# Kernel optimization log

Measured on AMD Instinct MI355X. Metric: run time of the kernel, lower is better.

## Reference

```python
import jax, jax.numpy as jnp
import numpy as np

N_TOKENS = 8192
D_MODEL = 1024
N_EXPERTS = 8
TOP_K = 2


def setup_inputs() -> dict:
    key = jax.random.key(0)
    ks = jax.random.split(key, 4)
    scale = 1.0 / np.sqrt(D_MODEL)
    x = jax.random.normal(ks[0], (N_TOKENS, D_MODEL), dtype=jnp.float32)
    gate_w = jax.random.uniform(ks[1], (N_EXPERTS, D_MODEL), jnp.float32, -scale, scale)
    expert_w = jax.random.uniform(ks[2], (N_EXPERTS, D_MODEL, D_MODEL), jnp.float32, -scale, scale)
    expert_b = jax.random.uniform(ks[3], (N_EXPERTS, D_MODEL), jnp.float32, -scale, scale)
    return {"x": x, "gate_w": gate_w, "expert_w": expert_w, "expert_b": expert_b}


def reference(x, gate_w, expert_w, expert_b):
    # Router: logits [N, E], softmax in fp32, top-k, renormalize over selected.
    router_logits = jnp.einsum('nd,ed->ne', x, gate_w)
    probs = jax.nn.softmax(router_logits.astype(jnp.float32), axis=1)
    rw, sel = jax.lax.top_k(probs, TOP_K)            # [N, K]
    rw = rw / jnp.sum(rw, axis=-1, keepdims=True)

    # Dense combine weights [N, E]: routing weight for selected experts, 0 else.
    n_idx = jnp.arange(x.shape[0])[:, None]
    w_dense = jnp.zeros((x.shape[0], N_EXPERTS), jnp.float32).at[n_idx, sel].set(rw)

    # Compute all experts for all tokens (vectorized equivalent of the
    # gather -> Linear -> weighted scatter-add loop; zero weight for
    # unselected experts reproduces the sparse dispatch exactly).
    # expert_w[e] is torch nn.Linear weight [out, in]: y = x @ W^T + b
    h = jnp.einsum('nd,ehd->neh', x, expert_w) + expert_b[None, :, :]  # [N, E, H]
    final = jnp.einsum('neh,ne->nh', h, w_dense.astype(x.dtype))
    return final, router_logits
```

## Files before the change

kernel.cpp:

```cpp
#include <hip/hip_runtime.h>
#include <hip/hip_bf16.h>
#include <stdint.h>

#define NT 8192
#define DM 1024
#define NE 8
#define MAX_TILES 160
#define SLOTS_MAX 17408
#define NKT (DM / 64)

typedef __bf16 bf16x8 __attribute__((ext_vector_type(8)));
typedef float f32x4 __attribute__((ext_vector_type(4)));

typedef const __attribute__((address_space(1))) void* gp_t;
typedef __attribute__((address_space(3))) void* lp_t;
#define GLDS(g, l) __builtin_amdgcn_global_load_lds((gp_t)(g), (lp_t)(l), 16, 0, 0)

__device__ inline unsigned short f2bf(float f) {
  unsigned int u = __float_as_uint(f);
  unsigned int r = (u + 0x7fffu + ((u >> 16) & 1u)) >> 16;
  return (unsigned short)r;
}
__device__ inline float bf2f(unsigned short u) {
  return __uint_as_float((unsigned int)u << 16);
}

__global__ void prep_kernel(const float* __restrict__ ew, unsigned short* __restrict__ wb,
                            const float* __restrict__ x, const float* __restrict__ gw,
                            float* __restrict__ logits, unsigned short* __restrict__ xb,
                            int* __restrict__ top2e, float* __restrict__ top2w,
                            int* __restrict__ pcount) {
  const int b = blockIdx.x;
  const int t = threadIdx.x;
  if (b < 4096) {
    size_t i = ((size_t)b * 256 + t) * 8;
    float4 a = *(const float4*)(ew + i);
    float4 c = *(const float4*)(ew + i + 4);
    union { unsigned short u[8]; uint4 v; } o;
    o.u[0] = f2bf(a.x); o.u[1] = f2bf(a.y); o.u[2] = f2bf(a.z); o.u[3] = f2bf(a.w);
    o.u[4] = f2bf(c.x); o.u[5] = f2bf(c.y); o.u[6] = f2bf(c.z); o.u[7] = f2bf(c.w);
    *(uint4*)(wb + i) = o.v;
    return;
  }
  __shared__ int lcnt[NE];
  if (t < NE) lcnt[t] = 0;
  __syncthreads();
  const int lane = t & 63;
  const int n = (b - 4096) * 4 + (t >> 6);
  const float* xr = x + (size_t)n * DM;
  float s[NE];
#pragma unroll
  for (int e = 0; e < NE; ++e) s[e] = 0.f;
  for (int c = lane; c < DM; c += 64) {
    float xv = xr[c];
    xb[(size_t)n * DM + c] = f2bf(xv);
#pragma unroll
    for (int e = 0; e < NE; ++e) s[e] += xv * gw[e * DM + c];
  }
#pragma unroll
  for (int e = 0; e < NE; ++e) {
#pragma unroll
    for (int off = 32; off > 0; off >>= 1) s[e] += __shfl_xor(s[e], off);
  }
  if (lane == 0) {
    float m = s[0];
#pragma unroll
    for (int e = 1; e < NE; ++e) m = fmaxf(m, s[e]);
    float p[NE];
#pragma unroll
    for (int e = 0; e < NE; ++e) {
      p[e] = __expf(s[e] - m);
      logits[(size_t)n * NE + e] = s[e];
    }
    int e1 = 0; float b1 = p[0];
#pragma unroll
    for (int e = 1; e < NE; ++e) if (p[e] > b1) { b1 = p[e]; e1 = e; }
    int e2 = -1; float b2 = -1.f;
#pragma unroll
    for (int e = 0; e < NE; ++e) if (e != e1 && p[e] > b2) { b2 = p[e]; e2 = e; }
    float inv = 1.f / (b1 + b2);
    top2e[n * 2 + 0] = e1; top2e[n * 2 + 1] = e2;
    top2w[n * 2 + 0] = b1 * inv; top2w[n * 2 + 1] = b2 * inv;
    atomicAdd(&lcnt[e1], 1);
    atomicAdd(&lcnt[e2], 1);
  }
  __syncthreads();
  if (t < NE) pcount[(b - 4096) * NE + t] = lcnt[t];
}

__global__ void plan_kernel(const int* __restrict__ pcount,
                            int* __restrict__ seg_base, int* __restrict__ counts2,
                            int* __restrict__ tile_e, int* __restrict__ tile_row,
                            int* __restrict__ n_tiles, int* __restrict__ slot_token) {
  __shared__ int lcnt[NE];
  __shared__ int sb[NE + 1], tb[NE + 1], cnt[NE];
  const int t = threadIdx.x;
  if (t < NE) lcnt[t] = 0;
  __syncthreads();
  int s[NE];
#pragma unroll
  for (int e = 0; e < NE; ++e) s[e] = 0;
#pragma unroll
  for (int i = 0; i < 8; ++i) {
    const int* p = pcount + (t + 256 * i) * NE;
#pragma unroll
    for (int e = 0; e < NE; ++e) s[e] += p[e];
  }
#pragma unroll
  for (int e = 0; e < NE; ++e) {
#pragma unroll
    for (int off = 32; off > 0; off >>= 1) s[e] += __shfl_xor(s[e], off);
  }
  if ((t & 63) == 0) {
#pragma unroll
    for (int e = 0; e < NE; ++e) atomicAdd(&lcnt[e], s[e]);
  }
  __syncthreads();
  if (t == 0) {
    int base = 0, tt = 0;
    for (int e = 0; e < NE; ++e) {
      sb[e] = base; tb[e] = tt;
      const int c = lcnt[e];
      cnt[e] = c;
      const int nt = (c + 127) >> 7;
      tt += nt;
      base += nt << 7;
    }
    sb[NE] = base; tb[NE] = tt;
    *n_tiles = tt;
  }
  __syncthreads();
  if (t <= NE) seg_base[t] = sb[t];
  if (t < NE) counts2[t] = 0;
  const int total = tb[NE];
  for (int i = t; i < total; i += 256) {
    int e = 0;
#pragma unroll
    for (int q = 0; q < NE; ++q) if (i >= tb[q + 1]) e = q + 1;
    tile_e[i] = e;
    tile_row[i] = sb[e] + (i - tb[e]) * 128;
  }
  for (int i = t; i < NE * 128; i += 256) {
    const int e = i >> 7, off = i & 127;
    const int pos = sb[e] + cnt[e] + off;
    if (pos < sb[e + 1]) slot_token[pos] = 0;
  }
}

__global__ void scatter_kernel(const int* __restrict__ top2e,
                               const int* __restrict__ seg_base, int* __restrict__ counts2,
                               int* __restrict__ slot_token, int* __restrict__ tok2slot) {
  __shared__ int lcnt[NE], lbase[NE];
  const int t = threadIdx.x;
  if (t < NE) lcnt[t] = 0;
  __syncthreads();
  const int n = blockIdx.x * 256 + t;
  const int e0 = top2e[n * 2 + 0], e1 = top2e[n * 2 + 1];
  const int p0 = atomicAdd(&lcnt[e0], 1);
  const int p1 = atomicAdd(&lcnt[e1], 1);
  __syncthreads();
  if (t < NE) lbase[t] = seg_base[t] + atomicAdd(&counts2[t], lcnt[t]);
  __syncthreads();
  const int q0 = lbase[e0] + p0, q1 = lbase[e1] + p1;
  slot_token[q0] = n; slot_token[q1] = n;
  tok2slot[n * 2 + 0] = q0;
  tok2slot[n * 2 + 1] = q1;
}

__global__ __launch_bounds__(256, 2) void moe_gemm_kernel(
    const unsigned short* __restrict__ xb,
    const unsigned short* __restrict__ wb,
    const float* __restrict__ bias,
    const int* __restrict__ slot_token,
    const int* __restrict__ tile_e, const int* __restrict__ tile_row,
    const int* __restrict__ n_tiles,
    unsigned short* __restrict__ y)
{
  const int bid = blockIdx.x;
  const int swz = (bid & 7) * 160 + (bid >> 3);
  const int bm = swz >> 3;
  const int bn = swz & 7;
  if (bm >= *n_tiles) return;
  const int e = tile_e[bm];
  const int row0 = tile_row[bm];
  const int n0 = bn * 128;

  __shared__ __align__(16) unsigned short lA[2][8192];
  __shared__ __align__(16) unsigned short lB[2][8192];

  const int t = threadIdx.x;
  const int lane = t & 63;
  const int w = t >> 6;
  const int wm = w >> 1, wn = w & 1;

  const int srow = t >> 3;
  const int ss = (t & 7) ^ (srow & 7);
  const unsigned short* asrc[4];
  const unsigned short* bsrc[4];
#pragma unroll
  for (int c = 0; c < 4; ++c) {
    const int lr = c * 32 + srow;
    const int tok = slot_token[row0 + lr];
    asrc[c] = xb + (size_t)tok * DM + ss * 8;
    bsrc[c] = wb + (size_t)e * DM * DM + (size_t)(n0 + lr) * DM + ss * 8;
  }

  f32x4 acc[4][4];
#pragma unroll
  for (int i = 0; i < 4; ++i)
#pragma unroll
    for (int j = 0; j < 4; ++j) acc[i][j] = (f32x4){0.f, 0.f, 0.f, 0.f};

  auto stage = [&](int buf, int kt) {
    const int ko = kt * 64;
#pragma unroll
    for (int c = 0; c < 4; ++c) {
      GLDS(asrc[c] + ko, &lA[buf][c * 2048 + w * 512]);
      GLDS(bsrc[c] + ko, &lB[buf][c * 2048 + w * 512]);
    }
  };

  stage(0, 0);
  stage(1, 1);

  for (int kt = 0; kt < NKT; ++kt) {
    if (kt < NKT - 1) {
      asm volatile("s_waitcnt vmcnt(8)" ::: "memory");
    } else {
      asm volatile("s_waitcnt vmcnt(0)" ::: "memory");
    }
    __builtin_amdgcn_sched_barrier(0);
    __builtin_amdgcn_s_barrier();

    const int cur = kt & 1;
    bf16x8 af[2][4], bf[2][4];
#pragma unroll
    for (int ks = 0; ks < 2; ++ks) {
      const int kb = ks * 64 + (lane >> 4) * 16;
#pragma unroll
      for (int mi = 0; mi < 4; ++mi) {
        const int row = wm * 64 + mi * 16 + (lane & 15);
        af[ks][mi] = *(const bf16x8*)((const char*)lA[cur] + row * 128 + (kb ^ ((row & 7) << 4)));
      }
#pragma unroll
      for (int ni = 0; ni < 4; ++ni) {
        const int row = wn * 64 + ni * 16 + (lane & 15);
        bf[ks][ni] = *(const bf16x8*)((const char*)lB[cur] + row * 128 + (kb ^ ((row & 7) << 4)));
      }
    }
    __builtin_amdgcn_s_setprio(1);
#pragma unroll
    for (int ks = 0; ks < 2; ++ks)
#pragma unroll
      for (int mi = 0; mi < 4; ++mi)
#pragma unroll
        for (int ni = 0; ni < 4; ++ni)
          acc[mi][ni] = __builtin_amdgcn_mfma_f32_16x16x32_bf16(af[ks][mi], bf[ks][ni], acc[mi][ni], 0, 0, 0);
    __builtin_amdgcn_s_setprio(0);

    __builtin_amdgcn_sched_barrier(0);
    __builtin_amdgcn_s_barrier();
    if (kt + 2 < NKT) stage(cur, kt + 2);
  }

  const int cgrp = lane >> 4, ccol = lane & 15;
  float bv[4];
#pragma unroll
  for (int ni = 0; ni < 4; ++ni)
    bv[ni] = bias[e * DM + n0 + wn * 64 + ni * 16 + ccol];
#pragma unroll
  for (int mi = 0; mi < 4; ++mi) {
#pragma unroll
    for (int j = 0; j < 4; ++j) {
      const int r = row0 + wm * 64 + mi * 16 + cgrp * 4 + j;
      unsigned short* yrow = y + (size_t)r * DM + n0 + wn * 64;
#pragma unroll
      for (int ni = 0; ni < 4; ++ni)
        yrow[ni * 16 + ccol] = f2bf(acc[mi][ni][j] + bv[ni]);
    }
  }
}

__global__ void combine_kernel(const unsigned short* __restrict__ y,
                               const int* __restrict__ tok2slot,
                               const float* __restrict__ top2w,
                               float* __restrict__ out) {
  const int n = blockIdx.x;
  const int c = threadIdx.x;
  const int s0 = tok2slot[n * 2 + 0], s1 = tok2slot[n * 2 + 1];
  const float w0 = top2w[n * 2 + 0], w1 = top2w[n * 2 + 1];
  ushort4 a = *(const ushort4*)(y + (size_t)s0 * DM + c * 4);
  ushort4 b = *(const ushort4*)(y + (size_t)s1 * DM + c * 4);
  float4 r;
  r.x = w0 * bf2f(a.x) + w1 * bf2f(b.x);
  r.y = w0 * bf2f(a.y) + w1 * bf2f(b.y);
  r.z = w0 * bf2f(a.z) + w1 * bf2f(b.z);
  r.w = w0 * bf2f(a.w) + w1 * bf2f(b.w);
  *(float4*)(out + (size_t)n * DM + c * 4) = r;
}

extern "C" void kernel_launch(void* const* d_in, const int* in_sizes, int n_in,
                              void* d_out, int out_size, void* d_ws, size_t ws_size,
                              hipStream_t stream) {
  const float* x  = (const float*)d_in[0];
  const float* gw = (const float*)d_in[1];
  const float* ew = (const float*)d_in[2];
  const float* eb = (const float*)d_in[3];
  float* out    = (float*)d_out;
  float* logits = out + (size_t)NT * DM;

  char* ws = (char*)d_ws;
  int*   counts2    = (int*)(ws + 64);
  int*   seg_base   = (int*)(ws + 128);
  int*   n_tiles    = (int*)(ws + 192);
  int*   tile_e     = (int*)(ws + 256);
  int*   tile_row   = (int*)(ws + 1024);
  int*   top2e      = (int*)(ws + 2048);
  float* top2w      = (float*)(ws + 67584);
  int*   slot_token = (int*)(ws + 133120);
  int*   tok2slot   = (int*)(ws + 202752);
  int*   pcount     = (int*)(ws + 268288);
  unsigned short* xb = (unsigned short*)(ws + 335872);
  unsigned short* wb = (unsigned short*)(ws + 335872 + 16777216);
  unsigned short* y  = (unsigned short*)(ws + 335872 + 2 * 16777216);

  prep_kernel<<<4096 + NT / 4, 256, 0, stream>>>(ew, wb, x, gw, logits, xb,
                                                 top2e, top2w, pcount);
  plan_kernel<<<1, 256, 0, stream>>>(pcount, seg_base, counts2, tile_e, tile_row,
                                     n_tiles, slot_token);
  scatter_kernel<<<NT / 256, 256, 0, stream>>>(top2e, seg_base, counts2, slot_token, tok2slot);
  moe_gemm_kernel<<<MAX_TILES * 8, 256, 0, stream>>>(xb, wb, eb, slot_token,
                                                     tile_e, tile_row, n_tiles, y);
  combine_kernel<<<NT, 256, 0, stream>>>(y, tok2slot, top2w, out);
}
```

Baseline: 99.10 us.

## Switch expert GEMM to 128x256 tiles with 32x32x16 MFMA and K=32 stages

```diff
diff --git a/kernel.cpp b/kernel.cpp
--- a/kernel.cpp
+++ b/kernel.cpp
@@ -7,10 +7,11 @@
 #define NE 8
 #define MAX_TILES 160
 #define SLOTS_MAX 17408
-#define NKT (DM / 64)
+#define NKT 32
 
 typedef __bf16 bf16x8 __attribute__((ext_vector_type(8)));
 typedef float f32x4 __attribute__((ext_vector_type(4)));
+typedef float f32x16 __attribute__((ext_vector_type(16)));
 
 typedef const __attribute__((address_space(1))) void* gp_t;
 typedef __attribute__((address_space(3))) void* lp_t;
@@ -177,55 +178,61 @@
     unsigned short* __restrict__ y)
 {
   const int bid = blockIdx.x;
-  const int swz = (bid & 7) * 160 + (bid >> 3);
-  const int bm = swz >> 3;
-  const int bn = swz & 7;
+  const int swz = (bid & 7) * 80 + (bid >> 3);
+  const int bm = swz >> 2;
+  const int bn = swz & 3;
   if (bm >= *n_tiles) return;
   const int e = tile_e[bm];
   const int row0 = tile_row[bm];
-  const int n0 = bn * 128;
-
-  __shared__ __align__(16) unsigned short lA[2][8192];
+  const int n0 = bn * 256;
+
+  __shared__ __align__(16) unsigned short lA[2][4096];
   __shared__ __align__(16) unsigned short lB[2][8192];
 
   const int t = threadIdx.x;
   const int lane = t & 63;
   const int w = t >> 6;
-  const int wm = w >> 1, wn = w & 1;
-
-  const int srow = t >> 3;
-  const int ss = (t & 7) ^ (srow & 7);
-  const unsigned short* asrc[4];
+
+  const int sS = (t & 7) ^ ((t >> 3) & 7);
+  const unsigned short* asrc[2];
   const unsigned short* bsrc[4];
 #pragma unroll
+  for (int c = 0; c < 2; ++c) {
+    const int lr = c * 64 + ((t >> 3) << 1) + (sS >> 2);
+    const int tok = slot_token[row0 + lr];
+    asrc[c] = xb + (size_t)tok * DM + (sS & 3) * 8;
+  }
+#pragma unroll
   for (int c = 0; c < 4; ++c) {
-    const int lr = c * 32 + srow;
-    const int tok = slot_token[row0 + lr];
-    asrc[c] = xb + (size_t)tok * DM + ss * 8;
-    bsrc[c] = wb + (size_t)e * DM * DM + (size_t)(n0 + lr) * DM + ss * 8;
-  }
-
-  f32x4 acc[4][4];
+    const int lr = c * 64 + ((t >> 3) << 1) + (sS >> 2);
+    bsrc[c] = wb + (size_t)e * DM * DM + (size_t)(n0 + lr) * DM + (sS & 3) * 8;
+  }
+
+  f32x16 acc[4][2];
 #pragma unroll
   for (int i = 0; i < 4; ++i)
 #pragma unroll
-    for (int j = 0; j < 4; ++j) acc[i][j] = (f32x4){0.f, 0.f, 0.f, 0.f};
+    for (int j = 0; j < 2; ++j)
+#pragma unroll
+      for (int v = 0; v < 16; ++v) acc[i][j][v] = 0.f;
 
   auto stage = [&](int buf, int kt) {
-    const int ko = kt * 64;
-#pragma unroll
-    for (int c = 0; c < 4; ++c) {
-      GLDS(asrc[c] + ko, &lA[buf][c * 2048 + w * 512]);
-      GLDS(bsrc[c] + ko, &lB[buf][c * 2048 + w * 512]);
-    }
+    const int ko = kt * 32;
+    GLDS(asrc[0] + ko, &lA[buf][t * 8]);
+    GLDS(asrc[1] + ko, &lA[buf][2048 + t * 8]);
+#pragma unroll
+    for (int c = 0; c < 4; ++c)
+      GLDS(bsrc[c] + ko, &lB[buf][c * 2048 + t * 8]);
   };
 
   stage(0, 0);
   stage(1, 1);
 
+  const int l31 = lane & 31;
+  const int khalf = lane >> 5;
   for (int kt = 0; kt < NKT; ++kt) {
     if (kt < NKT - 1) {
-      asm volatile("s_waitcnt vmcnt(8)" ::: "memory");
+      asm volatile("s_waitcnt vmcnt(6)" ::: "memory");
     } else {
       asm volatile("s_waitcnt vmcnt(0)" ::: "memory");
     }
@@ -233,29 +240,31 @@
     __builtin_amdgcn_s_barrier();
 
     const int cur = kt & 1;
-    bf16x8 af[2][4], bf[2][4];
-#pragma unroll
-    for (int ks = 0; ks < 2; ++ks) {
-      const int kb = ks * 64 + (lane >> 4) * 16;
-#pragma unroll
-      for (int mi = 0; mi < 4; ++mi) {
-        const int row = wm * 64 + mi * 16 + (lane & 15);
-        af[ks][mi] = *(const bf16x8*)((const char*)lA[cur] + row * 128 + (kb ^ ((row & 7) << 4)));
+    bf16x8 af[2][4], bf[2][2];
+#pragma unroll
+    for (int kg = 0; kg < 2; ++kg) {
+      const int q = kg * 2 + khalf;
+#pragma unroll
+      for (int mb = 0; mb < 4; ++mb) {
+        const int r = mb * 32 + l31;
+        const int off = (r >> 1) * 128 + (((((r & 1) << 2) | q) ^ ((r >> 1) & 7)) << 4);
+        af[kg][mb] = *(const bf16x8*)((const char*)lA[cur] + off);
       }
 #pragma unroll
-      for (int ni = 0; ni < 4; ++ni) {
-        const int row = wn * 64 + ni * 16 + (lane & 15);
-        bf[ks][ni] = *(const bf16x8*)((const char*)lB[cur] + row * 128 + (kb ^ ((row & 7) << 4)));
+      for (int nb = 0; nb < 2; ++nb) {
+        const int r = w * 64 + nb * 32 + l31;
+        const int off = (r >> 1) * 128 + (((((r & 1) << 2) | q) ^ ((r >> 1) & 7)) << 4);
+        bf[kg][nb] = *(const bf16x8*)((const char*)lB[cur] + off);
       }
     }
     __builtin_amdgcn_s_setprio(1);
 #pragma unroll
-    for (int ks = 0; ks < 2; ++ks)
-#pragma unroll
-      for (int mi = 0; mi < 4; ++mi)
-#pragma unroll
-        for (int ni = 0; ni < 4; ++ni)
-          acc[mi][ni] = __builtin_amdgcn_mfma_f32_16x16x32_bf16(af[ks][mi], bf[ks][ni], acc[mi][ni], 0, 0, 0);
+    for (int kg = 0; kg < 2; ++kg)
+#pragma unroll
+      for (int mb = 0; mb < 4; ++mb)
+#pragma unroll
+        for (int nb = 0; nb < 2; ++nb)
+          acc[mb][nb] = __builtin_amdgcn_mfma_f32_32x32x16_bf16(af[kg][mb], bf[kg][nb], acc[mb][nb], 0, 0, 0);
     __builtin_amdgcn_s_setprio(0);
 
     __builtin_amdgcn_sched_barrier(0);
@@ -263,20 +272,20 @@
     if (kt + 2 < NKT) stage(cur, kt + 2);
   }
 
-  const int cgrp = lane >> 4, ccol = lane & 15;
-  float bv[4];
-#pragma unroll
-  for (int ni = 0; ni < 4; ++ni)
-    bv[ni] = bias[e * DM + n0 + wn * 64 + ni * 16 + ccol];
-#pragma unroll
-  for (int mi = 0; mi < 4; ++mi) {
-#pragma unroll
-    for (int j = 0; j < 4; ++j) {
-      const int r = row0 + wm * 64 + mi * 16 + cgrp * 4 + j;
-      unsigned short* yrow = y + (size_t)r * DM + n0 + wn * 64;
-#pragma unroll
-      for (int ni = 0; ni < 4; ++ni)
-        yrow[ni * 16 + ccol] = f2bf(acc[mi][ni][j] + bv[ni]);
+  const int colb = n0 + w * 64;
+  float bv[2];
+#pragma unroll
+  for (int nb = 0; nb < 2; ++nb)
+    bv[nb] = bias[e * DM + colb + nb * 32 + l31];
+#pragma unroll
+  for (int mb = 0; mb < 4; ++mb) {
+#pragma unroll
+    for (int reg = 0; reg < 16; ++reg) {
+      const int r = row0 + mb * 32 + (reg & 3) + 8 * (reg >> 2) + 4 * khalf;
+      unsigned short* yrow = y + (size_t)r * DM + colb;
+#pragma unroll
+      for (int nb = 0; nb < 2; ++nb)
+        yrow[nb * 32 + l31] = f2bf(acc[mb][nb][reg] + bv[nb]);
     }
   }
 }
@@ -329,7 +338,7 @@
   plan_kernel<<<1, 256, 0, stream>>>(pcount, seg_base, counts2, tile_e, tile_row,
                                      n_tiles, slot_token);
   scatter_kernel<<<NT / 256, 256, 0, stream>>>(top2e, seg_base, counts2, slot_token, tok2slot);
-  moe_gemm_kernel<<<MAX_TILES * 8, 256, 0, stream>>>(xb, wb, eb, slot_token,
+  moe_gemm_kernel<<<MAX_TILES * 4, 256, 0, stream>>>(xb, wb, eb, slot_token,
                                                      tile_e, tile_row, n_tiles, y);
   combine_kernel<<<NT, 256, 0, stream>>>(y, tok2slot, top2w, out);
 }
```

Result: slower. 115.9 us (+17.0%).
